# Optimization experiments

Hardware: AMD Instinct MI355X
Metric: run time of the kernel (lower is better)

Reference implementation:

```python
import jax, jax.numpy as jnp
import numpy as np

TEMPERATURE = 0.5


def setup_inputs() -> dict:
    key = jax.random.key(0)
    ks = jax.random.split(key, 12)
    B, N, T = 128, 64, 256
    IN, H, OUT = N + T, 256, 128
    E = N * (N - 1) // 2  # 2016 upper-tri edges per graph
    total_edges = B * E
    inp = {
        "x_topology": jax.random.normal(ks[0], (B, N, N), jnp.float32),
        "x_temporal": jax.random.normal(ks[1], (B, N, T), jnp.float32),
        "gumbel_u": jax.random.uniform(ks[2], (total_edges,), jnp.float32, 1e-6, 1.0),
        # GNNLayer linear
        "W_gnn": jax.random.normal(ks[3], (IN, H), jnp.float32) / np.sqrt(IN),
        "b_gnn": jnp.zeros((H,), jnp.float32),
        # edge heads (input dim 2*H)
        "W_mean": jax.random.normal(ks[4], (2 * H, OUT), jnp.float32) / np.sqrt(2 * H),
        "b_mean": jnp.zeros((OUT,), jnp.float32),
        "W_var": jax.random.normal(ks[5], (2 * H, OUT), jnp.float32) / np.sqrt(2 * H),
        "b_var": jnp.zeros((OUT,), jnp.float32),
        "W_w": jax.random.normal(ks[6], (2 * H, 1), jnp.float32) / np.sqrt(2 * H),
        "b_w": jnp.zeros((1,), jnp.float32),
    }
    return inp


def reference(x_topology, x_temporal, gumbel_u, W_gnn, b_gnn,
              W_mean, b_mean, W_var, b_var, W_w, b_w):
    B, N, _ = x_topology.shape
    T = x_temporal.shape[-1]
    # Upper-triangular fully-connected edge index (no self loops), batched with node offsets.
    row, col = jnp.triu_indices(N, k=1)          # [E]
    E = row.shape[0]
    offs = (jnp.arange(B) * N)[:, None]          # [B,1]
    src = (row[None, :] + offs).reshape(-1)       # [B*E]
    dst = (col[None, :] + offs).reshape(-1)       # [B*E]

    # Node features: concat topology + temporal, flatten batch of graphs.
    x = jnp.concatenate([x_topology, x_temporal], axis=-1).reshape(B * N, N + T)

    # Mean aggregation (PyG aggr='mean'): messages x[src] scattered to dst; 0 for isolated nodes.
    msg_sum = jax.ops.segment_sum(x[src], dst, num_segments=B * N)      # [B*N, N+T]
    cnt = jax.ops.segment_sum(jnp.ones_like(src, x.dtype), dst, num_segments=B * N)
    agg = jnp.where(cnt[:, None] > 0, msg_sum / jnp.maximum(cnt, 1.0)[:, None], 0.0)

    h = jax.nn.relu(agg @ W_gnn + b_gnn)          # [B*N, H]

    # Edge MLP heads on gathered [src||dst] embeddings.
    ef = jnp.concatenate([h[src], h[dst]], axis=-1)        # [B*E, 2H]
    mean = ef @ W_mean + b_mean                             # [B*E, OUT]
    variance = jax.nn.softplus(ef @ W_var + b_var) + 1e-6   # [B*E, OUT]
    weight = jax.nn.sigmoid((ef @ W_w + b_w)[:, 0])          # [B*E]

    # Gumbel-softmax over the flattened edge-weight vector (dim=-1 of a 1-D tensor).
    g = -jnp.log(-jnp.log(gumbel_u))
    gumbel_w = jax.nn.softmax((weight + g) / TEMPERATURE, axis=-1)

    # Gaussian similarity per edge, scatter into dense adjacency.
    sim = jnp.exp(-0.5 * jnp.mean(mean ** 2 / (variance + 1e-8), axis=-1))
    edge_w = sim * gumbel_w                                  # [B*E]

    b_idx = jnp.repeat(jnp.arange(B), E)
    adj = jnp.zeros((B, N, N), x.dtype).at[b_idx, jnp.tile(row, B), jnp.tile(col, B)].set(edge_w)
    return adj
```

## Files before the change

### kernel.cpp

```cpp
#include <hip/hip_runtime.h>
#include <hip/hip_bf16.h>
#include <math.h>

#define Bg   128
#define Nn   64
#define Tt   256
#define INF  320
#define Hd   256
#define OUTD 128
#define Ee   2016
#define TOTE (Bg*Ee)
#define SCOLS 576
#define MROWS 8192

#define RSQRT_LN2 1.2011224087864498f
#define LOG2E     1.4426950408889634f
#define EPS_T     1.45719e-6f

typedef __attribute__((ext_vector_type(8))) short bf16x8;
typedef __attribute__((ext_vector_type(4))) float f32x4;

static __device__ __forceinline__ ushort f2bf(float v) {
    __hip_bfloat16 h = __float2bfloat16(v);
    return *(ushort*)&h;
}

#define CVT_N (INF * Hd)
#define PACK_N (Hd * SCOLS)
__global__ void k_prep(const float* __restrict__ Wg, const float* __restrict__ Wm,
                       const float* __restrict__ Wv, const float* __restrict__ Ww,
                       const float* __restrict__ bm, const float* __restrict__ bv,
                       const float* __restrict__ bw,
                       ushort* __restrict__ WgbT, ushort* __restrict__ WcatT,
                       float* __restrict__ ebias, unsigned* __restrict__ red) {
    int idx = blockIdx.x * 256 + threadIdx.x;
    if (idx == 0) { red[0] = 0u; red[1] = 0u; }
    if (idx < CVT_N) {
        int n = idx / INF, k = idx - n * INF;
        WgbT[idx] = f2bf(Wg[k * Hd + n]);
        return;
    }
    idx -= CVT_N;
    if (idx < PACK_N) {
        int n = idx / Hd, k = idx - n * Hd;
        float v = 0.f;
        if (n < 128)       v = Wm[k * 128 + n];
        else if (n < 256)  v = Wm[(256 + k) * 128 + (n - 128)];
        else if (n < 384)  v = Wv[k * 128 + (n - 256)];
        else if (n < 512)  v = Wv[(256 + k) * 128 + (n - 384)];
        else if (n == 512) v = Ww[k];
        else if (n == 513) v = Ww[256 + k];
        WcatT[idx] = f2bf(v);
        return;
    }
    idx -= PACK_N;
    if (idx >= SCOLS) return;
    float e = 0.f;
    if (idx < 128)                    e = bm[idx];
    else if (idx >= 256 && idx < 384) e = bv[idx - 256];
    else if (idx == 512)              e = bw[0];
    ebias[idx] = e;
}

__global__ __launch_bounds__(256) void k_agg(const float* __restrict__ topo,
                                             const float* __restrict__ temp,
                                             ushort* __restrict__ agg) {
    __shared__ float T[64 * 65];
    const int b = blockIdx.x, ft = blockIdx.y;
    const int tid = threadIdx.x;
    const int row = tid >> 2, seg = tid & 3;
    const float* src = (ft == 0) ? (topo + (size_t)(b * Nn + row) * Nn)
                                 : (temp + (size_t)(b * Nn + row) * Tt + (ft - 1) * 64);
    #pragma unroll
    for (int i = 0; i < 4; ++i) {
        float4 v = *(const float4*)(src + seg * 16 + i * 4);
        float* d = &T[row * 65 + seg * 16 + i * 4];
        d[0] = v.x; d[1] = v.y; d[2] = v.z; d[3] = v.w;
    }
    __syncthreads();
    const int w = tid >> 6, lane = tid & 63;
    #pragma unroll
    for (int k = 0; k < 16; ++k) {
        int f = w * 16 + k;
        float x = T[lane * 65 + f];
        float incl = x;
        #pragma unroll
        for (int o = 1; o < 64; o <<= 1) {
            float t = __shfl_up(incl, o);
            if (lane >= o) incl += t;
        }
        float excl = incl - x;
        T[lane * 65 + f] = lane ? excl * __builtin_amdgcn_rcpf((float)lane) : 0.f;
    }
    __syncthreads();
    const int node = tid >> 2, f0 = (tid & 3) * 16;
    ushort tmp[16];
    #pragma unroll
    for (int i = 0; i < 16; ++i) tmp[i] = f2bf(T[node * 65 + f0 + i]);
    ushort* dst = agg + (size_t)(b * Nn + node) * INF + ft * 64 + f0;
    *(uint4*)dst = *(uint4*)tmp;
    *(uint4*)(dst + 8) = *(uint4*)(tmp + 8);
}

__global__ __launch_bounds__(256) void k_gemm_mfma(const ushort* __restrict__ A,
                                                   const ushort* __restrict__ BT,
                                                   const float* __restrict__ bias,
                                                   ushort* __restrict__ Cb,
                                                   float* __restrict__ Cf,
                                                   int N, int K, int relu, int transC,
                                                   int edgeScale) {
    __shared__ ushort Asl[64 * 72];
    __shared__ ushort Bsl[64 * 72];
    const int tid = threadIdx.x;
    const int w = tid >> 6, lane = tid & 63;
    const int quad = lane >> 4, r16 = lane & 15;
    const int m0 = blockIdx.y * 64, n0 = blockIdx.x * 64;
    const int row = tid >> 2, seg = tid & 3;
    f32x4 acc[4] = {};

    for (int k0 = 0; k0 < K; k0 += 64) {
        const ushort* ap = A + (size_t)(m0 + row) * K + k0 + seg * 16;
        uint4 a0 = ((const uint4*)ap)[0];
        uint4 a1 = ((const uint4*)ap)[1];
        *(uint4*)(Asl + row * 72 + seg * 16)     = a0;
        *(uint4*)(Asl + row * 72 + seg * 16 + 8) = a1;
        const ushort* bp = BT + (size_t)(n0 + row) * K + k0 + seg * 16;
        uint4 b0 = ((const uint4*)bp)[0];
        uint4 b1 = ((const uint4*)bp)[1];
        *(uint4*)(Bsl + row * 72 + seg * 16)     = b0;
        *(uint4*)(Bsl + row * 72 + seg * 16 + 8) = b1;
        __syncthreads();

        bf16x8 af0 = *(const bf16x8*)(Asl + (w * 16 + r16) * 72 + quad * 8);
        bf16x8 af1 = *(const bf16x8*)(Asl + (w * 16 + r16) * 72 + 32 + quad * 8);
        #pragma unroll
        for (int ns = 0; ns < 4; ++ns) {
            bf16x8 bf0 = *(const bf16x8*)(Bsl + (ns * 16 + r16) * 72 + quad * 8);
            bf16x8 bf1 = *(const bf16x8*)(Bsl + (ns * 16 + r16) * 72 + 32 + quad * 8);
            acc[ns] = __builtin_amdgcn_mfma_f32_16x16x32_bf16(af0, bf0, acc[ns], 0, 0, 0);
            acc[ns] = __builtin_amdgcn_mfma_f32_16x16x32_bf16(af1, bf1, acc[ns], 0, 0, 0);
        }
        __syncthreads();
    }

    const int row0 = m0 + w * 16 + quad * 4;
    #pragma unroll
    for (int ns = 0; ns < 4; ++ns) {
        f32x4 a = acc[ns];
        int col = n0 + ns * 16 + r16;
        float bb = bias ? bias[col] : 0.f;
        float vv[4];
        #pragma unroll
        for (int i = 0; i < 4; ++i) {
            float v = a[i] + bb;
            if (relu) v = fmaxf(v, 0.f);
            vv[i] = v;
        }
        if (transC) {
            if (edgeScale) {
                float s = (col < 256) ? RSQRT_LN2 : (col < 512 ? LOG2E : 1.f);
                #pragma unroll
                for (int i = 0; i < 4; ++i) vv[i] *= s;
            }
            *(float4*)(Cf + (size_t)col * MROWS + row0) = make_float4(vv[0], vv[1], vv[2], vv[3]);
        } else {
            #pragma unroll
            for (int i = 0; i < 4; ++i) {
                int row2 = row0 + i;
                if (Cb) Cb[(size_t)row2 * N + col] = f2bf(vv[i]);
                else    Cf[(size_t)row2 * N + col] = vv[i];
            }
        }
    }
}

static __device__ __forceinline__ float eterm(float pm, float qm, float pv, float qv) {
    float m = pm + qm;
    float y = pv + qv;
    float e = __builtin_amdgcn_exp2f(-__builtin_fabsf(y));
    float t = fmaxf(y, 0.f) + __builtin_amdgcn_logf(1.f + e)
            + EPS_T;
    return m * m * __builtin_amdgcn_rcpf(t);
}

__global__ __launch_bounds__(256, 8) void k_edge4(const float* __restrict__ ST,
                                                  const float* __restrict__ gu,
                                                  float* __restrict__ numer,
                                                  unsigned* __restrict__ red) {
    __shared__ float L[4][16][68];
    __shared__ float sred[4];
    const int bid = blockIdx.x;
    const int xcd = bid & 7, k = bid >> 3;
    const int b = xcd * 16 + k / 10;
    const int p = k - (k / 10) * 10;
    const int G0v[10] = {0,0,0,0,1,1,1,2,2,3};
    const int G1v[10] = {0,1,2,3,1,2,3,2,3,3};
    const int g0 = G0v[p], g1 = G1v[p];
    const int tid = threadIdx.x;

    int i, j;
    bool valid;
    if (g0 != g1) {
        i = tid >> 4; j = tid & 15; valid = true;
    } else {
        valid = tid < 120;
        int ii = 0, rr = tid;
        if (valid) { while (rr >= 15 - ii) { rr -= 15 - ii; ++ii; } }
        i = valid ? ii : 0;
        j = valid ? (ii + 1 + rr) : 1;
    }

    const int c = tid >> 2, nq = tid & 3;
    float acc = 0.f;
    #pragma unroll
    for (int h = 0; h < 2; ++h) {
        if (h) __syncthreads();
        #pragma unroll
        for (int arr = 0; arr < 4; ++arr) {
            const int g = (arr & 1) ? g1 : g0;
            float4 v = *(const float4*)&ST[(size_t)((arr << 7) + (h << 6) + c) * MROWS
                                           + b * 64 + (g << 4) + (nq << 2)];
            L[arr][nq * 4 + 0][c] = v.x;
            L[arr][nq * 4 + 1][c] = v.y;
            L[arr][nq * 4 + 2][c] = v.z;
            L[arr][nq * 4 + 3][c] = v.w;
        }
        __syncthreads();
        if (valid) {
            #pragma unroll 4
            for (int t = 0; t < 64; t += 4) {
                float4 mi = *(const float4*)&L[0][i][t];
                float4 mj = *(const float4*)&L[1][j][t];
                float4 vi = *(const float4*)&L[2][i][t];
                float4 vj = *(const float4*)&L[3][j][t];
                acc += eterm(mi.x, mj.x, vi.x, vj.x);
                acc += eterm(mi.y, mj.y, vi.y, vj.y);
                acc += eterm(mi.z, mj.z, vi.z, vj.z);
                acc += eterm(mi.w, mj.w, vi.w, vj.w);
            }
        }
    }

    const int ni = g0 * 16 + i, nj = g1 * 16 + j;
    float en = 0.f;
    if (valid) {
        int e = b * Ee + (ni * (127 - ni)) / 2 + (nj - ni - 1);
        float se = __expf(acc * (-1.f / 256.f));
        float wr = ST[(size_t)512 * MROWS + b * 64 + ni]
                 + ST[(size_t)513 * MROWS + b * 64 + nj];
        float w  = __builtin_amdgcn_rcpf(1.f + __expf(-wr));
        float g  = -__logf(-__logf(gu[e]));
        en = __expf((w + g) * 2.0f);
        numer[e] = se * en;
    }
    #pragma unroll
    for (int o = 32; o; o >>= 1) en += __shfl_down(en, o);
    if ((tid & 63) == 0) sred[tid >> 6] = en;
    __syncthreads();
    if (tid == 0) atomicAdd((float*)&red[1], sred[0] + sred[1] + sred[2] + sred[3]);
}

__global__ void k_out(const float* __restrict__ numer, const unsigned* __restrict__ red,
                      float* __restrict__ out) {
    int idx = blockIdx.x * 256 + threadIdx.x;
    if (idx >= Bg * Nn * Nn) return;
    int b = idx >> 12;
    int rem = idx & 4095;
    int r = rem >> 6, c = rem & 63;
    float v = 0.f;
    if (c > r) {
        int e = b * Ee + (r * (127 - r)) / 2 + (c - r - 1);
        float Sinv = __builtin_amdgcn_rcpf(((const float*)red)[1]);
        v = numer[e] * Sinv;
    }
    out[idx] = v;
}

extern "C" void kernel_launch(void* const* d_in, const int* in_sizes, int n_in,
                              void* d_out, int out_size, void* d_ws, size_t ws_size,
                              hipStream_t stream) {
    const float* topo = (const float*)d_in[0];
    const float* temp = (const float*)d_in[1];
    const float* gu   = (const float*)d_in[2];
    const float* Wg   = (const float*)d_in[3];
    const float* bg   = (const float*)d_in[4];
    const float* Wm   = (const float*)d_in[5];
    const float* bm   = (const float*)d_in[6];
    const float* Wv   = (const float*)d_in[7];
    const float* bv   = (const float*)d_in[8];
    const float* Ww   = (const float*)d_in[9];
    const float* bw   = (const float*)d_in[10];
    float* out = (float*)d_out;

    char* ws = (char*)d_ws;
    size_t off = 0;
    auto carve = [&](size_t bytes) { char* p = ws + off; off = (off + bytes + 255) & ~(size_t)255; return p; };

    char*   r1    = carve((size_t)SCOLS * MROWS * 4);
    float*  ST    = (float*)r1;
    ushort* aggb  = (ushort*)r1;
    ushort* hb    = (ushort*)carve((size_t)MROWS * Hd * 2);
    ushort* WgbT  = (ushort*)carve((size_t)INF * Hd * 2);
    ushort* WcatT = (ushort*)carve((size_t)Hd * SCOLS * 2);
    float*  ebias = (float*)carve((size_t)SCOLS * 4);
    float*  numer = (float*)carve((size_t)TOTE * 4);
    unsigned* red = (unsigned*)carve(256);

    k_prep<<<(CVT_N + PACK_N + SCOLS + 255) / 256, 256, 0, stream>>>(
        Wg, Wm, Wv, Ww, bm, bv, bw, WgbT, WcatT, ebias, red);
    k_agg<<<dim3(Bg, INF / 64), 256, 0, stream>>>(topo, temp, aggb);
    k_gemm_mfma<<<dim3(Hd / 64, MROWS / 64), 256, 0, stream>>>(
        aggb, WgbT, bg, hb, nullptr, Hd, INF, 1, 0, 0);
    k_gemm_mfma<<<dim3(SCOLS / 64, MROWS / 64), 256, 0, stream>>>(
        hb, WcatT, ebias, nullptr, ST, SCOLS, Hd, 0, 1, 1);
    k_edge4<<<Bg * 10, 256, 0, stream>>>(ST, gu, numer, red);
    k_out<<<(Bg * Nn * Nn + 255) / 256, 256, 0, stream>>>(numer, red, out);
}
```

Measured before the change: 135.9 us.

## Precompute exp of variance halves and restructure edge kernel with 2x2 register tiling

```diff
diff --git a/kernel.cpp b/kernel.cpp
--- a/kernel.cpp
+++ b/kernel.cpp
@@ -158,9 +158,14 @@
         }
         if (transC) {
             if (edgeScale) {
-                float s = (col < 256) ? RSQRT_LN2 : (col < 512 ? LOG2E : 1.f);
-                #pragma unroll
-                for (int i = 0; i < 4; ++i) vv[i] *= s;
+                if (col < 256) {
+                    #pragma unroll
+                    for (int i = 0; i < 4; ++i) vv[i] *= RSQRT_LN2;
+                } else if (col < 512) {
+                    #pragma unroll
+                    for (int i = 0; i < 4; ++i)
+                        vv[i] = __builtin_amdgcn_exp2f(vv[i] * LOG2E);
+                }
             }
             *(float4*)(Cf + (size_t)col * MROWS + row0) = make_float4(vv[0], vv[1], vv[2], vv[3]);
         } else {
@@ -174,94 +179,123 @@
     }
 }
 
-static __device__ __forceinline__ float eterm(float pm, float qm, float pv, float qv) {
-    float m = pm + qm;
-    float y = pv + qv;
-    float e = __builtin_amdgcn_exp2f(-__builtin_fabsf(y));
-    float t = fmaxf(y, 0.f) + __builtin_amdgcn_logf(1.f + e)
-            + EPS_T;
+static __device__ __forceinline__ float et(float mA, float mB, float eA, float eB) {
+    float m = mA + mB;
+    float E = eA * eB;
+    float t = __builtin_amdgcn_logf(1.f + E) + EPS_T;
     return m * m * __builtin_amdgcn_rcpf(t);
 }
 
-__global__ __launch_bounds__(256, 8) void k_edge4(const float* __restrict__ ST,
-                                                  const float* __restrict__ gu,
-                                                  float* __restrict__ numer,
-                                                  unsigned* __restrict__ red) {
-    __shared__ float L[4][16][68];
-    __shared__ float sred[4];
+__global__ __launch_bounds__(512, 4) void k_edge5(const float* __restrict__ ST,
+                                                  float* __restrict__ accp) {
+    __shared__ float L[4][64][36];
     const int bid = blockIdx.x;
-    const int xcd = bid & 7, k = bid >> 3;
-    const int b = xcd * 16 + k / 10;
-    const int p = k - (k / 10) * 10;
-    const int G0v[10] = {0,0,0,0,1,1,1,2,2,3};
-    const int G1v[10] = {0,1,2,3,1,2,3,2,3,3};
-    const int g0 = G0v[p], g1 = G1v[p];
+    const int b = bid >> 2, oc = bid & 3;
     const int tid = threadIdx.x;
 
-    int i, j;
-    bool valid;
-    if (g0 != g1) {
-        i = tid >> 4; j = tid & 15; valid = true;
-    } else {
-        valid = tid < 120;
-        int ii = 0, rr = tid;
-        if (valid) { while (rr >= 15 - ii) { rr -= 15 - ii; ++ii; } }
-        i = valid ? ii : 0;
-        j = valid ? (ii + 1 + rr) : 1;
-    }
-
-    const int c = tid >> 2, nq = tid & 3;
-    float acc = 0.f;
-    #pragma unroll
-    for (int h = 0; h < 2; ++h) {
-        if (h) __syncthreads();
+    {
+        const int c = (tid >> 4) & 31, q = tid & 15, n = q << 2;
+        const int s0 = c ^ ((((n    ) >> 1) & 7) << 2);
+        const int s1 = c ^ ((((n + 1) >> 1) & 7) << 2);
+        const int s2 = c ^ ((((n + 2) >> 1) & 7) << 2);
+        const int s3 = c ^ ((((n + 3) >> 1) & 7) << 2);
         #pragma unroll
         for (int arr = 0; arr < 4; ++arr) {
-            const int g = (arr & 1) ? g1 : g0;
-            float4 v = *(const float4*)&ST[(size_t)((arr << 7) + (h << 6) + c) * MROWS
-                                           + b * 64 + (g << 4) + (nq << 2)];
-            L[arr][nq * 4 + 0][c] = v.x;
-            L[arr][nq * 4 + 1][c] = v.y;
-            L[arr][nq * 4 + 2][c] = v.z;
-            L[arr][nq * 4 + 3][c] = v.w;
-        }
-        __syncthreads();
-        if (valid) {
-            #pragma unroll 4
-            for (int t = 0; t < 64; t += 4) {
-                float4 mi = *(const float4*)&L[0][i][t];
-                float4 mj = *(const float4*)&L[1][j][t];
-                float4 vi = *(const float4*)&L[2][i][t];
-                float4 vj = *(const float4*)&L[3][j][t];
-                acc += eterm(mi.x, mj.x, vi.x, vj.x);
-                acc += eterm(mi.y, mj.y, vi.y, vj.y);
-                acc += eterm(mi.z, mj.z, vi.z, vj.z);
-                acc += eterm(mi.w, mj.w, vi.w, vj.w);
-            }
-        }
-    }
-
-    const int ni = g0 * 16 + i, nj = g1 * 16 + j;
+            float4 v = *(const float4*)&ST[(size_t)(arr * 128 + oc * 32 + c) * MROWS
+                                           + b * 64 + n];
+            L[arr][n + 0][s0] = v.x;
+            L[arr][n + 1][s1] = v.y;
+            L[arr][n + 2][s2] = v.z;
+            L[arr][n + 3][s3] = v.w;
+        }
+    }
+
+    const bool strict = tid < 496;
+    int ri0, ri1, rj0, rj1;
+    if (strict) {
+        int rr = tid, ci = 0;
+        while (rr >= 31 - ci) { rr -= 31 - ci; ++ci; }
+        int cj = ci + 1 + rr;
+        ri0 = 2 * ci; ri1 = ri0 + 1;
+        rj0 = 2 * cj; rj1 = rj0 + 1;
+    } else {
+        int d0 = (tid - 496) * 2, d1 = d0 + 1;
+        ri0 = 2 * d0; rj0 = ri0 + 1;
+        ri1 = 2 * d1; rj1 = ri1 + 1;
+    }
+    const float* M0 = &L[0][ri0][0]; const float* M1 = &L[0][ri1][0];
+    const float* N0 = &L[1][rj0][0]; const float* N1 = &L[1][rj1][0];
+    const float* E0 = &L[2][ri0][0]; const float* E1 = &L[2][ri1][0];
+    const float* F0 = &L[3][rj0][0]; const float* F1 = &L[3][rj1][0];
+    const int si0 = ((ri0 >> 1) & 7) << 2, si1 = ((ri1 >> 1) & 7) << 2;
+    const int sj0 = ((rj0 >> 1) & 7) << 2, sj1 = ((rj1 >> 1) & 7) << 2;
+
+    __syncthreads();
+
+    float a00 = 0.f, a01 = 0.f, a10 = 0.f, a11 = 0.f;
+    #pragma unroll 4
+    for (int t = 0; t < 32; t += 4) {
+        float4 m0 = *(const float4*)(M0 + (t ^ si0));
+        float4 m1 = *(const float4*)(M1 + (t ^ si1));
+        float4 n0 = *(const float4*)(N0 + (t ^ sj0));
+        float4 n1 = *(const float4*)(N1 + (t ^ sj1));
+        float4 e0 = *(const float4*)(E0 + (t ^ si0));
+        float4 e1 = *(const float4*)(E1 + (t ^ si1));
+        float4 f0 = *(const float4*)(F0 + (t ^ sj0));
+        float4 f1 = *(const float4*)(F1 + (t ^ sj1));
+        a00 += et(m0.x,n0.x,e0.x,f0.x) + et(m0.y,n0.y,e0.y,f0.y)
+             + et(m0.z,n0.z,e0.z,f0.z) + et(m0.w,n0.w,e0.w,f0.w);
+        a11 += et(m1.x,n1.x,e1.x,f1.x) + et(m1.y,n1.y,e1.y,f1.y)
+             + et(m1.z,n1.z,e1.z,f1.z) + et(m1.w,n1.w,e1.w,f1.w);
+        if (strict) {
+            a01 += et(m0.x,n1.x,e0.x,f1.x) + et(m0.y,n1.y,e0.y,f1.y)
+                 + et(m0.z,n1.z,e0.z,f1.z) + et(m0.w,n1.w,e0.w,f1.w);
+            a10 += et(m1.x,n0.x,e1.x,f0.x) + et(m1.y,n0.y,e1.y,f0.y)
+                 + et(m1.z,n0.z,e1.z,f0.z) + et(m1.w,n0.w,e1.w,f0.w);
+        }
+    }
+
+    float* ap = accp + (size_t)oc * TOTE + (size_t)b * Ee;
+    if (strict) {
+        int e0i = (ri0 * (127 - ri0)) / 2 + (rj0 - ri0 - 1);
+        int e1i = (ri1 * (127 - ri1)) / 2 + (rj0 - ri1 - 1);
+        ap[e0i] = a00; ap[e0i + 1] = a01;
+        ap[e1i] = a10; ap[e1i + 1] = a11;
+    } else {
+        ap[(ri0 * (127 - ri0)) / 2] = a00;
+        ap[(ri1 * (127 - ri1)) / 2] = a11;
+    }
+}
+
+__global__ __launch_bounds__(256) void k_den(const float* __restrict__ ST,
+                                             const float* __restrict__ gu,
+                                             float* __restrict__ numer,
+                                             unsigned* __restrict__ red) {
+    __shared__ float sred[4];
+    const int tid = threadIdx.x;
+    int idx = blockIdx.x * 256 + tid;
+    int b = idx >> 12, rem = idx & 4095;
+    int r = rem >> 6, c = rem & 63;
     float en = 0.f;
-    if (valid) {
-        int e = b * Ee + (ni * (127 - ni)) / 2 + (nj - ni - 1);
-        float se = __expf(acc * (-1.f / 256.f));
-        float wr = ST[(size_t)512 * MROWS + b * 64 + ni]
-                 + ST[(size_t)513 * MROWS + b * 64 + nj];
+    if (c > r) {
+        int e = b * Ee + (r * (127 - r)) / 2 + (c - r - 1);
+        float wr = ST[(size_t)512 * MROWS + b * 64 + r]
+                 + ST[(size_t)513 * MROWS + b * 64 + c];
         float w  = __builtin_amdgcn_rcpf(1.f + __expf(-wr));
         float g  = -__logf(-__logf(gu[e]));
         en = __expf((w + g) * 2.0f);
-        numer[e] = se * en;
-    }
-    #pragma unroll
-    for (int o = 32; o; o >>= 1) en += __shfl_down(en, o);
-    if ((tid & 63) == 0) sred[tid >> 6] = en;
+        numer[e] = en;
+    }
+    float s = en;
+    #pragma unroll
+    for (int o = 32; o; o >>= 1) s += __shfl_down(s, o);
+    if ((tid & 63) == 0) sred[tid >> 6] = s;
     __syncthreads();
     if (tid == 0) atomicAdd((float*)&red[1], sred[0] + sred[1] + sred[2] + sred[3]);
 }
 
-__global__ void k_out(const float* __restrict__ numer, const unsigned* __restrict__ red,
-                      float* __restrict__ out) {
+__global__ void k_out(const float* __restrict__ accp, const float* __restrict__ numer,
+                      const unsigned* __restrict__ red, float* __restrict__ out) {
     int idx = blockIdx.x * 256 + threadIdx.x;
     if (idx >= Bg * Nn * Nn) return;
     int b = idx >> 12;
@@ -270,8 +304,10 @@
     float v = 0.f;
     if (c > r) {
         int e = b * Ee + (r * (127 - r)) / 2 + (c - r - 1);
+        float a = accp[e] + accp[TOTE + e] + accp[2 * TOTE + e] + accp[3 * TOTE + e];
+        float se = __expf(a * (-1.f / 256.f));
         float Sinv = __builtin_amdgcn_rcpf(((const float*)red)[1]);
-        v = numer[e] * Sinv;
+        v = se * numer[e] * Sinv;
     }
     out[idx] = v;
 }
@@ -304,6 +340,7 @@
     ushort* WcatT = (ushort*)carve((size_t)Hd * SCOLS * 2);
     float*  ebias = (float*)carve((size_t)SCOLS * 4);
     float*  numer = (float*)carve((size_t)TOTE * 4);
+    float*  accp  = (float*)carve((size_t)4 * TOTE * 4);
     unsigned* red = (unsigned*)carve(256);
 
     k_prep<<<(CVT_N + PACK_N + SCOLS + 255) / 256, 256, 0, stream>>>(
@@ -313,6 +350,7 @@
         aggb, WgbT, bg, hb, nullptr, Hd, INF, 1, 0, 0);
     k_gemm_mfma<<<dim3(SCOLS / 64, MROWS / 64), 256, 0, stream>>>(
         hb, WcatT, ebias, nullptr, ST, SCOLS, Hd, 0, 1, 1);
-    k_edge4<<<Bg * 10, 256, 0, stream>>>(ST, gu, numer, red);
-    k_out<<<(Bg * Nn * Nn + 255) / 256, 256, 0, stream>>>(numer, red, out);
-}
+    k_edge5<<<Bg * 4, 512, 0, stream>>>(ST, accp);
+    k_den<<<(Bg * Nn * Nn) / 256, 256, 0, stream>>>(ST, gu, numer, red);
+    k_out<<<(Bg * Nn * Nn + 255) / 256, 256, 0, stream>>>(accp, numer, red, out);
+}
```

Measured after the change: 177.4 us. 30.6% more time.
